# Optimization experiments

Measured on AMD Instinct MI355X. Metric: run time of the kernel, lower is better.

The kernel has to match this reference:

```python
import jax, jax.numpy as jnp
import numpy as np

N = 256   # num_atoms
V = 64    # v_dim
E = 64    # e_dim
S = 16    # num_sims
H = 16    # hidden size hard-coded in the module


def setup_inputs() -> dict:
    key = jax.random.key(0)
    ks = jax.random.split(key, 12)
    # edge index lists equivalent to the one-hot rel_rec / rel_send matmuls
    off_diag = np.ones((N, N), dtype=np.float32) - np.eye(N, dtype=np.float32)
    send_np, recv_np = np.where(off_diag)  # rows=senders ([0]), cols=receivers ([1])
    def w(k, shape):
        fan_in = shape[0]
        return (jax.random.normal(k, shape, jnp.float32) / np.sqrt(fan_in)).astype(jnp.float32)
    return {
        "t": jnp.zeros((), jnp.float32),
        "v0": jax.random.normal(ks[0], (S, N, V), jnp.float32),
        "e0": jax.random.normal(ks[1], (S, N, N - 1, E), jnp.float32),
        "wv1": w(ks[2], (E, H)), "bv1": jnp.zeros((H,), jnp.float32),
        "wv2": w(ks[3], (H, V)), "bv2": jnp.zeros((V,), jnp.float32),
        "we1": w(ks[4], (2 * V, H)), "be1": jnp.zeros((H,), jnp.float32),
        "we2": w(ks[5], (H, E)), "be2": jnp.zeros((E,), jnp.float32),
        "recv_idx": jnp.asarray(recv_np, jnp.int32),
        "send_idx": jnp.asarray(send_np, jnp.int32),
    }


def reference(t, v0, e0, wv1, bv1, wv2, bv2, we1, be1, we2, be2, recv_idx, send_idx):
    # dv = mlp_v(sum_j e0[:, :, j, :])  -> [S, N, V]
    ev = jnp.sum(e0, axis=2)                               # [S, N, E]
    dv = jnp.tanh(ev @ wv1 + bv1) @ wv2 + bv2              # [S, N, V]

    # node2edge: one-hot matmuls == gathers along the node axis
    receivers = v0[:, recv_idx, :]                          # [S, N*(N-1), V]
    senders = v0[:, send_idx, :]                            # [S, N*(N-1), V]
    edges = jnp.concatenate([receivers, senders], axis=-1)  # [S, N*(N-1), 2V]

    de = jnp.tanh(edges @ we1 + be1) @ we2 + be2            # [S, N*(N-1), E]
    de = de.reshape(de.shape[0], N, N - 1, de.shape[-1])    # [S, N, N-1, E]
    return (dv, de)
```

## Files before the change

### kernel.cpp

```cpp
#include <hip/hip_runtime.h>
#include <cstddef>

#define NN 256
#define VD 64
#define ED 64
#define SD 16
#define HD 16
#define EPS 65280
#define DE_TILES 16320
#define DV_BLOCKS 4096

typedef float f32x4 __attribute__((ext_vector_type(4)));

__device__ __forceinline__ float fast_tanh(float x) {
    float e = __expf(2.0f * x);
    float r = __builtin_amdgcn_rcpf(e + 1.0f);
    return 1.0f - 2.0f * r;
}

__global__ __launch_bounds__(256) void precompute_ab(
    const float* __restrict__ v0, const float* __restrict__ we1,
    float* __restrict__ a_tab, float* __restrict__ b_tab) {
    int t = threadIdx.x;
    int i = t & 15;
    int nl = t >> 4;
    int node = blockIdx.x * 16 + nl;
    const float* vrow = v0 + (size_t)node * VD;
    float a = 0.f, b = 0.f;
    #pragma unroll
    for (int k = 0; k < VD; ++k) {
        float x = vrow[k];
        a += x * we1[k * HD + i];
        b += x * we1[(VD + k) * HD + i];
    }
    a_tab[node * HD + i] = a;
    b_tab[node * HD + i] = b;
}

__global__ __launch_bounds__(256) void fused_dv_de(
    const float* __restrict__ e0,
    const float* __restrict__ wv1, const float* __restrict__ bv1,
    const float* __restrict__ wv2, const float* __restrict__ bv2,
    const float* __restrict__ a_tab, const float* __restrict__ b_tab,
    const float* __restrict__ we2, const float* __restrict__ be1,
    const float* __restrict__ be2,
    const int* __restrict__ recv_idx, const int* __restrict__ send_idx,
    float* __restrict__ dv_out, float* __restrict__ de_out) {
    __shared__ float smem[1344];
    int bid = blockIdx.x;
    int q = bid / 5;
    int r = bid - q * 5;
    int t = threadIdx.x;

    if (r == 4) {
        float* red  = smem;
        float* ev_s = smem + 1024;
        float* h_s  = smem + 1088;
        int node = q;
        const float* base = e0 + (size_t)node * 255 * ED;
        int c = t & 15;
        int g = t >> 4;
        f32x4 acc = (f32x4){0.f, 0.f, 0.f, 0.f};
        for (int j = g; j < 255; j += 16) {
            const f32x4 v = __builtin_nontemporal_load(
                (const f32x4*)(base + (size_t)j * ED + c * 4));
            acc += v;
        }
        *(f32x4*)(red + g * 64 + c * 4) = acc;
        __syncthreads();
        if (t < 64) {
            float s = 0.f;
            #pragma unroll
            for (int gg = 0; gg < 16; ++gg) s += red[gg * 64 + t];
            ev_s[t] = s;
        }
        __syncthreads();
        if (t < 16) {
            float ah = bv1[t];
            #pragma unroll
            for (int e = 0; e < 64; ++e) ah += ev_s[e] * wv1[e * HD + t];
            h_s[t] = fast_tanh(ah);
        }
        __syncthreads();
        if (t < 64) {
            float o = bv2[t];
            #pragma unroll
            for (int i = 0; i < HD; ++i) o += h_s[i] * wv2[i * VD + t];
            dv_out[(size_t)node * VD + t] = o;
        }
    } else {
        int dt = q * 4 + r;
        if (dt >= DE_TILES) return;
        int s = dt / 1020;
        int tile = dt - s * 1020;
        float* h_s = smem;

        int p = t & 63;
        int iq = t >> 6;
        int eg = tile * 64 + p;

        int rr = recv_idx[eg];
        int sd = send_idx[eg];
        const float4 av = *(const float4*)(a_tab + ((s << 8) + rr) * HD + iq * 4);
        const float4 bv = *(const float4*)(b_tab + ((s << 8) + sd) * HD + iq * 4);
        const float4 b1 = *(const float4*)(be1 + iq * 4);
        float4 hv;
        hv.x = fast_tanh(av.x + bv.x + b1.x);
        hv.y = fast_tanh(av.y + bv.y + b1.y);
        hv.z = fast_tanh(av.z + bv.z + b1.z);
        hv.w = fast_tanh(av.w + bv.w + b1.w);
        *(float4*)(h_s + p * 20 + iq * 4) = hv;

        int v = t & 63;
        float w2[16];
        #pragma unroll
        for (int i = 0; i < HD; ++i) w2[i] = we2[i * ED + v];
        float bias = be2[v];
        __syncthreads();

        int w = t >> 6;
        size_t outbase = ((size_t)s * EPS + (size_t)tile * 64) * ED;
        for (int pp = w * 16; pp < w * 16 + 16; ++pp) {
            const float* hp = h_s + pp * 20;
            float o = bias;
            #pragma unroll
            for (int i = 0; i < HD; i += 4) {
                float4 h4 = *(const float4*)(hp + i);
                o += h4.x * w2[i] + h4.y * w2[i + 1] + h4.z * w2[i + 2] + h4.w * w2[i + 3];
            }
            __builtin_nontemporal_store(o, de_out + outbase + (size_t)pp * ED + v);
        }
    }
}

extern "C" void kernel_launch(void* const* d_in, const int* in_sizes, int n_in,
                              void* d_out, int out_size, void* d_ws, size_t ws_size,
                              hipStream_t stream) {
    const float* v0   = (const float*)d_in[1];
    const float* e0   = (const float*)d_in[2];
    const float* wv1  = (const float*)d_in[3];
    const float* bv1  = (const float*)d_in[4];
    const float* wv2  = (const float*)d_in[5];
    const float* bv2  = (const float*)d_in[6];
    const float* we1  = (const float*)d_in[7];
    const float* be1  = (const float*)d_in[8];
    const float* we2  = (const float*)d_in[9];
    const float* be2  = (const float*)d_in[10];
    const int* recv_idx = (const int*)d_in[11];
    const int* send_idx = (const int*)d_in[12];

    float* dv_out = (float*)d_out;
    float* de_out = dv_out + (size_t)SD * NN * VD;
    float* a_tab  = (float*)d_ws;
    float* b_tab  = a_tab + 4096 * HD;

    precompute_ab<<<256, 256, 0, stream>>>(v0, we1, a_tab, b_tab);
    fused_dv_de<<<DV_BLOCKS * 5, 256, 0, stream>>>(
        e0, wv1, bv1, wv2, bv2, a_tab, b_tab, we2, be1, be2,
        recv_idx, send_idx, dv_out, de_out);
}
```

Before: 453.7 us.

## Compute de per sender row with implicit indices instead of gathered 64-edge tiles

Each de block now handles all 255 edges of one sender node and derives the receiver index arithmetically (j = pp + (pp >= i)) instead of loading recv_idx/send_idx. The sender's b_tab row is loaded once per block, and the block count drops from 5 per node to 2 per node. This removes the index-array reads and some per-block setup, in exchange for a larger shared-memory tile (5100 floats) and longer per-wave store loops. It relies on the edge lists being the fixed off-diagonal ordering.

Result: no change. 461.0 us (+1.6%).

```diff
diff --git a/kernel.cpp b/kernel.cpp
--- a/kernel.cpp
+++ b/kernel.cpp
@@ -7,8 +7,8 @@
 #define SD 16
 #define HD 16
 #define EPS 65280
-#define DE_TILES 16320
 #define DV_BLOCKS 4096
+#define DE_ROWS 4096
 
 typedef float f32x4 __attribute__((ext_vector_type(4)));
 
@@ -44,15 +44,14 @@
     const float* __restrict__ a_tab, const float* __restrict__ b_tab,
     const float* __restrict__ we2, const float* __restrict__ be1,
     const float* __restrict__ be2,
-    const int* __restrict__ recv_idx, const int* __restrict__ send_idx,
     float* __restrict__ dv_out, float* __restrict__ de_out) {
-    __shared__ float smem[1344];
+    __shared__ float smem[5100];
     int bid = blockIdx.x;
-    int q = bid / 5;
-    int r = bid - q * 5;
+    int q = bid >> 1;
+    int r = bid & 1;
     int t = threadIdx.x;
 
-    if (r == 4) {
+    if (r == 1) {
         float* red  = smem;
         float* ev_s = smem + 1024;
         float* h_s  = smem + 1088;
@@ -89,44 +88,44 @@
             dv_out[(size_t)node * VD + t] = o;
         }
     } else {
-        int dt = q * 4 + r;
-        if (dt >= DE_TILES) return;
-        int s = dt / 1020;
-        int tile = dt - s * 1020;
+        int s = q >> 8;
+        int i = q & 255;
         float* h_s = smem;
 
         int p = t & 63;
         int iq = t >> 6;
-        int eg = tile * 64 + p;
 
-        int rr = recv_idx[eg];
-        int sd = send_idx[eg];
-        const float4 av = *(const float4*)(a_tab + ((s << 8) + rr) * HD + iq * 4);
-        const float4 bv = *(const float4*)(b_tab + ((s << 8) + sd) * HD + iq * 4);
         const float4 b1 = *(const float4*)(be1 + iq * 4);
-        float4 hv;
-        hv.x = fast_tanh(av.x + bv.x + b1.x);
-        hv.y = fast_tanh(av.y + bv.y + b1.y);
-        hv.z = fast_tanh(av.z + bv.z + b1.z);
-        hv.w = fast_tanh(av.w + bv.w + b1.w);
-        *(float4*)(h_s + p * 20 + iq * 4) = hv;
+        const float4 bv = *(const float4*)(b_tab + ((s << 8) + i) * HD + iq * 4);
+        #pragma unroll
+        for (int pp = p; pp < 255; pp += 64) {
+            int j = pp + (pp >= i);
+            const float4 av = *(const float4*)(a_tab + ((s << 8) + j) * HD + iq * 4);
+            float4 hv;
+            hv.x = fast_tanh(av.x + bv.x + b1.x);
+            hv.y = fast_tanh(av.y + bv.y + b1.y);
+            hv.z = fast_tanh(av.z + bv.z + b1.z);
+            hv.w = fast_tanh(av.w + bv.w + b1.w);
+            *(float4*)(h_s + pp * 20 + iq * 4) = hv;
+        }
 
         int v = t & 63;
         float w2[16];
         #pragma unroll
-        for (int i = 0; i < HD; ++i) w2[i] = we2[i * ED + v];
+        for (int ii = 0; ii < HD; ++ii) w2[ii] = we2[ii * ED + v];
         float bias = be2[v];
         __syncthreads();
 
         int w = t >> 6;
-        size_t outbase = ((size_t)s * EPS + (size_t)tile * 64) * ED;
-        for (int pp = w * 16; pp < w * 16 + 16; ++pp) {
+        size_t outbase = ((size_t)s * EPS + (size_t)i * 255) * ED;
+        int ppend = (w == 3) ? 255 : (w * 64 + 64);
+        for (int pp = w * 64; pp < ppend; ++pp) {
             const float* hp = h_s + pp * 20;
             float o = bias;
             #pragma unroll
-            for (int i = 0; i < HD; i += 4) {
-                float4 h4 = *(const float4*)(hp + i);
-                o += h4.x * w2[i] + h4.y * w2[i + 1] + h4.z * w2[i + 2] + h4.w * w2[i + 3];
+            for (int ii = 0; ii < HD; ii += 4) {
+                float4 h4 = *(const float4*)(hp + ii);
+                o += h4.x * w2[ii] + h4.y * w2[ii + 1] + h4.z * w2[ii + 2] + h4.w * w2[ii + 3];
             }
             __builtin_nontemporal_store(o, de_out + outbase + (size_t)pp * ED + v);
         }
@@ -146,8 +145,6 @@
     const float* be1  = (const float*)d_in[8];
     const float* we2  = (const float*)d_in[9];
     const float* be2  = (const float*)d_in[10];
-    const int* recv_idx = (const int*)d_in[11];
-    const int* send_idx = (const int*)d_in[12];
 
     float* dv_out = (float*)d_out;
     float* de_out = dv_out + (size_t)SD * NN * VD;
@@ -155,7 +152,7 @@
     float* b_tab  = a_tab + 4096 * HD;
 
     precompute_ab<<<256, 256, 0, stream>>>(v0, we1, a_tab, b_tab);
-    fused_dv_de<<<DV_BLOCKS * 5, 256, 0, stream>>>(
+    fused_dv_de<<<DV_BLOCKS * 2, 256, 0, stream>>>(
         e0, wv1, bv1, wv2, bv2, a_tab, b_tab, we2, be1, be2,
-        recv_idx, send_idx, dv_out, de_out);
+        dv_out, de_out);
 }
```
